# Optimization experiments

Measured on AMD Instinct MI355X. Metric: run time of the kernel, lower is better.

The kernel has to match this reference:

```python
import jax, jax.numpy as jnp
import numpy as np

S = 128           # seq_len
B = 256           # input_bits (bits per token, also neurons per head)
H = 16            # num_heads
NB = 12           # n_bits_per_neuron -> LUT size 2^12
PB = 7            # relative-position bits = ceil(log2(max_seq_len))
HEAD_IN = 2 * B + PB   # concat(query, key, rel_pos_bits) = 519
THRESH = H // 2


def setup_inputs() -> dict:
    key = jax.random.key(0)
    k1, k2, k3 = jax.random.split(key, 3)
    tokens = jax.random.randint(k1, (S, B), 0, 2, dtype=jnp.int32)           # binary token bits
    memory = jax.random.normal(k2, (H, B, 2 ** NB), dtype=jnp.float32)       # RAM LUT contents per head/neuron
    connections = jax.random.randint(k3, (H, B, NB), 0, HEAD_IN, dtype=jnp.int32)  # per-neuron input-bit wiring
    return {"tokens": tokens, "memory": memory, "connections": connections}


def reference(tokens, memory, connections):
    idx = jnp.arange(S)
    rel = idx[:, None] - idx[None, :]                         # [S,S] i - j
    mask = (rel >= 0).astype(jnp.int32)                        # causal mask (j <= i)
    relc = jnp.clip(rel, 0, S - 1)
    # relative-distance binary encoding, LSB first: [S,S,PB]
    pos_bits = ((relc[..., None] >> jnp.arange(PB)) & 1).astype(jnp.int32)
    q = jnp.broadcast_to(tokens[:, None, :], (S, S, B))
    k = jnp.broadcast_to(tokens[None, :, :], (S, S, B))
    head_in = jnp.concatenate([q, k, pos_bits], axis=-1)       # [S,S,HEAD_IN]
    # RAM address per (query i, key j, head h, neuron n): pack NB wired bits, LSB first
    addr = jnp.zeros((S, S, H, B), dtype=jnp.int32)
    for b in range(NB):  # tiny fixed loop over bit planes, fully vectorized over S,S,H,B
        addr = addr + (head_in[..., connections[:, :, b]] << b)
    # LUT gather: memory[h, n, addr] -> [S,S,H,B]
    h_idx = jnp.arange(H)[:, None]
    n_idx = jnp.arange(B)[None, :]
    vals = memory[h_idx, n_idx, addr]
    bits = (vals > 0.0).astype(jnp.int32)                      # RAM neuron output bit
    # XOR accumulation over attended keys == masked sum mod 2: [S,H,B]
    head_res = jnp.sum(bits * mask[:, :, None, None], axis=1) % 2
    # majority vote across heads per bit
    ones_count = jnp.sum(head_res, axis=1)                     # [S,B]
    return (ones_count > THRESH).astype(jnp.int32)
```

## Files before the change

### kernel.cpp

```cpp
#include <hip/hip_runtime.h>


#define S 128
#define B 256
#define H 16
#define NB 12

__device__ __forceinline__ unsigned sig(unsigned x) {
    return x ^ ((x >> 3) & 0x70u) ^ ((x >> 6) & 0x70u);
}

#define TW(c) ((((c) & 3) << 1) + ((c) >> 7))
#define TP(c) (((c) >> 2) & 31)

__global__ __launch_bounds__(256) void pack_kernel(
    const int* __restrict__ tokens,
    unsigned* __restrict__ tokP)
{
    const int wid  = threadIdx.x >> 6;
    const int lane = threadIdx.x & 63;
    const int4* tp = (const int4*)tokens;
    #pragma unroll
    for (int r = 0; r < 4; ++r) {
        int i = blockIdx.x * 16 + wid * 4 + r;
        int4 x = tp[i * 64 + lane];
        unsigned long long B0 = __ballot((x.x & 1) != 0);
        unsigned long long B1 = __ballot((x.y & 1) != 0);
        unsigned long long B2 = __ballot((x.z & 1) != 0);
        unsigned long long B3 = __ballot((x.w & 1) != 0);
        int c = lane >> 1;
        unsigned long long s01 = (c & 1) ? B1 : B0;
        unsigned long long s23 = (c & 1) ? B3 : B2;
        unsigned long long s   = (c & 2) ? s23 : s01;
        unsigned word = (lane & 1) ? (unsigned)(s >> 32) : (unsigned)s;
        if (lane < 8) tokP[lane * 128 + i] = word;
    }
}

__global__ __launch_bounds__(256, 8) void softram_kernel(
    const unsigned* __restrict__ tokP,
    const float* __restrict__ memory,
    const int* __restrict__ connections,
    unsigned long long* __restrict__ pres)
{
    const int tid  = threadIdx.x;
    const int wid  = tid >> 6;
    const int rs   = wid >> 1;
    const int sub  = wid & 1;
    const int r    = blockIdx.x * 2 + rs;
    const int lane = tid & 63;

    __shared__ __align__(16) unsigned char      bytetab[2][4096];
    __shared__ __align__(16) unsigned int       tokT[8 * S];
    __shared__ __align__(16) unsigned short     akT[2][S];
    __shared__ __align__(16) unsigned short     apt[2][S];
    __shared__ __align__(16) unsigned short     aqs[2][S];
    __shared__ __align__(16) unsigned long long wsh[2][64];
    __shared__ unsigned long long baseS[2];
    __shared__ unsigned long long fbu[2];

    unsigned char* __restrict__ bt = bytetab[rs];

    const float4* mp = (const float4*)(memory + ((size_t)r << 12));
    float4 va[4];
    #pragma unroll
    for (int t = 0; t < 4; ++t) va[t] = mp[lane + 64 * (sub * 8 + t)];

    int c_l = (lane < NB) ? connections[(size_t)r * NB + lane] : 0;
    int cb[NB];
    #pragma unroll
    for (int b = 0; b < NB; ++b)
        cb[b] = __builtin_amdgcn_readfirstlane(__shfl(c_l, b));

    unsigned qmask = 0, kmask = 0, pmask = 0;
    #pragma unroll
    for (int b = 0; b < NB; ++b) {
        qmask |= (unsigned)(cb[b] < 256) << b;
        kmask |= (unsigned)(cb[b] >= 256 && cb[b] < 512) << b;
        pmask |= (unsigned)(cb[b] >= 512) << b;
    }
    const int qb = __popc(qmask);
    const int kb = __popc(kmask);
    const bool fast = (pmask == 0);

    ((int4*)tokT)[tid] = ((const int4*)tokP)[tid];
    __syncthreads();

    const int ii = sub * 64 + lane;
    unsigned qcls = 0;
    if (fast) {
        unsigned qc = 0, kc = 0;
        int qn = 0, kn = 0;
        #pragma unroll
        for (int b = 0; b < NB; ++b) {
            int c = cb[b];
            if (c < 256) {
                qc |= ((tokT[TW(c) * S + ii] >> TP(c)) & 1u) << qn;
                ++qn;
            } else {
                int c2 = c - 256;
                kc |= ((tokT[TW(c2) * S + ii] >> TP(c2)) & 1u) << kn;
                ++kn;
            }
        }
        akT[rs][ii] = (unsigned short)kc;
        qcls = qc;
    } else {
        unsigned aq = 0, ak = 0, ap = 0;
        #pragma unroll
        for (int b = 0; b < NB; ++b) {
            int c = cb[b];
            if (c < 256) {
                aq |= ((tokT[TW(c) * S + ii] >> TP(c)) & 1u) << b;
            } else if (c < 512) {
                int c2 = c - 256;
                ak |= ((tokT[TW(c2) * S + ii] >> TP(c2)) & 1u) << b;
            } else {
                ap |= (((unsigned)ii >> (c - 512)) & 1u) << b;
            }
        }
        akT[rs][ii] = (unsigned short)sig(ak);
        apt[rs][ii] = (unsigned short)sig(ap);
        aqs[rs][ii] = (unsigned short)sig(aq);
        qcls = sig(aq);
    }

    #pragma unroll
    for (int t = 0; t < 8; ++t) {
        float4 v = va[t & 3];
        if (t + 4 < 8) va[t & 3] = mp[lane + 64 * (sub * 8 + t + 4)];
        unsigned w = (unsigned)(v.x > 0.f)
                   | ((unsigned)(v.y > 0.f) << 8)
                   | ((unsigned)(v.z > 0.f) << 16)
                   | ((unsigned)(v.w > 0.f) << 24);
        *(unsigned*)&bt[sig(4u * (unsigned)(lane + 64 * (sub * 8 + t)))] = w;
    }
    __syncthreads();

    unsigned long long rpart = 0;
    unsigned long long Wfull = 0;
    unsigned long long Vreg  = 0;
    unsigned Creg = 0;
    unsigned acc_fb = 0;

    if (fast) {
        const bool formA = (qb <= 6);
        const int SBITS  = formA ? qb : kb;
        unsigned apl = 0, aul = 0;
        {
            int scnt = 0, lcnt = 0;
            #pragma unroll
            for (int b = 0; b < NB; ++b) {
                int c = cb[b];
                bool isS = formA ? (c < 256) : (c >= 256);
                if (isS) {
                    apl |= (((unsigned)lane >> scnt) & 1u) << b;
                    ++scnt;
                } else {
                    int p = SBITS + lcnt;
                    if (p < 6) apl |= (((unsigned)lane >> p) & 1u) << b;
                    else       aul |= (((unsigned)lane >> (p - 6)) & 1u) << b;
                    ++lcnt;
                }
            }
        }
        const unsigned spl  = sig(apl);
        const unsigned saul = sig(aul);
        unsigned Wlo = 0, Whi = 0;
        #pragma unroll 8
        for (int k = 0; k < 32; ++k) {
            int it = sub * 32 + k;
            unsigned sau  = (unsigned)__builtin_amdgcn_readlane((int)saul, it);
            unsigned bitv = bt[sau ^ spl] & 1u;
            unsigned long long Bm = __ballot(bitv != 0u);
            Wlo = (lane == it) ? (unsigned)Bm : Wlo;
            Whi = (lane == it) ? (unsigned)(Bm >> 32) : Whi;
        }
        if ((lane >> 5) == sub)
            wsh[rs][lane] = ((unsigned long long)Whi << 32) | Wlo;
    } else {
        if (sub == 0) {
            const unsigned aqv0 = qcls;
            const unsigned aqvU = aqs[rs][64 + lane];
            unsigned acc0 = 0, accP = 0;
            for (int s8 = 0; s8 < 8; ++s8) {
                uint4 uk = *(const uint4*)&akT[rs][s8 * 8];
                #pragma unroll
                for (int t = 0; t < 8; ++t) {
                    int j = s8 * 8 + t;
                    unsigned w = ((const unsigned*)&uk)[t >> 1];
                    unsigned akv = (w >> ((t & 1) * 16)) & 0xffffu;
                    int d0 = lane - j;
                    unsigned v0 = bt[aqv0 ^ akv ^ (unsigned)apt[rs][d0 & 127]] & 1u;
                    acc0 ^= (d0 >= 0) ? v0 : 0u;
                    int d1 = lane + 64 - j;
                    unsigned v1 = bt[aqvU ^ akv ^ (unsigned)apt[rs][d1]] & 1u;
                    accP ^= v1;
                }
            }
            rpart = __ballot(acc0 != 0u);
            unsigned long long up = __ballot(accP != 0u);
            if (lane == 0) fbu[rs] = up;
        } else {
            const unsigned aqv1 = qcls;
            unsigned acc1 = 0;
            for (int s8 = 8; s8 < 16; ++s8) {
                uint4 uk = *(const uint4*)&akT[rs][s8 * 8];
                #pragma unroll
                for (int t = 0; t < 8; ++t) {
                    int j = s8 * 8 + t;
                    unsigned w = ((const unsigned*)&uk)[t >> 1];
                    unsigned akv = (w >> ((t & 1) * 16)) & 0xffffu;
                    int d1 = lane + 64 - j;
                    unsigned v1 = bt[aqv1 ^ akv ^ (unsigned)apt[rs][d1 & 127]] & 1u;
                    acc1 ^= (d1 >= 0) ? v1 : 0u;
                }
            }
            acc_fb = acc1;
        }
    }
    __syncthreads();

    if (fast) {
        Wfull = wsh[rs][lane];
        const bool formA = (qb <= 6);
        if (formA) {
            unsigned kcls = akT[rs][ii];
            unsigned g0 = kcls << qb;
            unsigned long long V = __shfl(Wfull, (int)(g0 >> 6)) >> (g0 & 63u);
            #pragma unroll
            for (int d = 1; d < 64; d <<= 1) {
                unsigned long long u = __shfl_up(V, (unsigned)d);
                V ^= (lane >= d) ? u : 0ull;
            }
            if (sub == 0) {
                rpart = __ballot(((V >> qcls) & 1ull) != 0ull);
                unsigned long long Ab = __shfl(V, 63);
                if (lane == 0) baseS[rs] = Ab;
            } else {
                Vreg = V;
            }
        } else {
            unsigned kcls = akT[rs][ii];
            unsigned C = 1u << kcls;
            #pragma unroll
            for (int d = 1; d < 64; d <<= 1) {
                unsigned u = __shfl_up(C, (unsigned)d);
                C ^= (lane >= d) ? u : 0u;
            }
            if (sub == 0) {
                unsigned g0a = qcls << kb;
                unsigned W0 = (unsigned)(__shfl(Wfull, (int)(g0a >> 6)) >> (g0a & 63u));
                rpart = __ballot((__popc(W0 & C) & 1) != 0);
                unsigned Cb = __shfl(C, 63);
                if (lane == 0) baseS[rs] = (unsigned long long)Cb;
            } else {
                Creg = C;
            }
        }
    } else if (sub == 1) {
        unsigned long long up = fbu[rs];
        acc_fb ^= (unsigned)((up >> lane) & 1ull);
        rpart = __ballot(acc_fb != 0u);
    }
    __syncthreads();

    if (fast && sub == 1) {
        const bool formA = (qb <= 6);
        if (formA) {
            unsigned long long V1 = Vreg ^ baseS[rs];
            rpart = __ballot(((V1 >> qcls) & 1ull) != 0ull);
        } else {
            unsigned C1 = Creg ^ (unsigned)baseS[rs];
            unsigned g0b = qcls << kb;
            unsigned W1 = (unsigned)(__shfl(Wfull, (int)(g0b >> 6)) >> (g0b & 63u));
            rpart = __ballot((__popc(W1 & C1) & 1) != 0);
        }
    }

    if (lane == 0) pres[(size_t)r * 2 + sub] = rpart;
}

__global__ __launch_bounds__(128) void vote_kernel(
    const unsigned long long* __restrict__ pres,
    int* __restrict__ out)
{
    const int n = blockIdx.x;
    const int i = threadIdx.x;
    const int w = i >> 6, b = i & 63;
    int tot = 0;
    #pragma unroll
    for (int h = 0; h < H; ++h)
        tot += (int)((pres[(size_t)(h * 256 + n) * 2 + w] >> b) & 1ull);
    out[i * B + n] = (tot > (H / 2)) ? 1 : 0;
}

extern "C" void kernel_launch(void* const* d_in, const int* in_sizes, int n_in,
                              void* d_out, int out_size, void* d_ws, size_t ws_size,
                              hipStream_t stream) {
    const int*   tokens      = (const int*)d_in[0];
    const float* memory      = (const float*)d_in[1];
    const int*   connections = (const int*)d_in[2];
    int*         out         = (int*)d_out;
    unsigned long long* pres = (unsigned long long*)d_ws;
    unsigned*           tokP = (unsigned*)((char*)d_ws + (64u << 10));
    (void)in_sizes; (void)n_in; (void)out_size; (void)ws_size;

    pack_kernel<<<8, 256, 0, stream>>>(tokens, tokP);
    softram_kernel<<<2048, 256, 0, stream>>>(tokP, memory, connections, pres);
    vote_kernel<<<B, 128, 0, stream>>>(pres, out);
}
```

Baseline: 108.3 us.

## Process two neuron pairs per block with upfront prefetch and LDS-only barriers

Each softram block now handles four neurons (two per wave pair, processed one after the other), so the grid is halved. The tokT staging and its setup are amortised over twice the work. Both neurons' LUT float4 data and connection lists are loaded up front, so the second neuron's global loads overlap the first neuron's compute. __syncthreads is replaced by a barrier that waits only on LDS/scalar counters. The cost is more VGPRs for the 16 prefetched float4s and lower occupancy, since launch bounds drop from 8 to 4 waves per EU.

New measurement: 111.6 us. 1.03x slower.

```diff
diff --git a/kernel.cpp b/kernel.cpp
--- a/kernel.cpp
+++ b/kernel.cpp
@@ -12,6 +12,12 @@
 
 #define TW(c) ((((c) & 3) << 1) + ((c) >> 7))
 #define TP(c) (((c) >> 2) & 31)
+
+#define LGKM_BAR() do { \
+    asm volatile("s_waitcnt lgkmcnt(0)" ::: "memory"); \
+    __builtin_amdgcn_s_barrier(); \
+    __builtin_amdgcn_sched_barrier(0); \
+} while (0)
 
 __global__ __launch_bounds__(256) void pack_kernel(
     const int* __restrict__ tokens,
@@ -37,7 +43,7 @@
     }
 }
 
-__global__ __launch_bounds__(256, 8) void softram_kernel(
+__global__ __launch_bounds__(256, 4) void softram_kernel(
     const unsigned* __restrict__ tokP,
     const float* __restrict__ memory,
     const int* __restrict__ connections,
@@ -47,8 +53,10 @@
     const int wid  = tid >> 6;
     const int rs   = wid >> 1;
     const int sub  = wid & 1;
-    const int r    = blockIdx.x * 2 + rs;
     const int lane = tid & 63;
+    const int r0   = blockIdx.x * 4 + rs;
+    const int r1   = blockIdx.x * 4 + 2 + rs;
+    const int ii   = sub * 64 + lane;
 
     __shared__ __align__(16) unsigned char      bytetab[2][4096];
     __shared__ __align__(16) unsigned int       tokT[8 * S];
@@ -59,226 +67,234 @@
     __shared__ unsigned long long baseS[2];
     __shared__ unsigned long long fbu[2];
 
-    unsigned char* __restrict__ bt = bytetab[rs];
-
-    const float4* mp = (const float4*)(memory + ((size_t)r << 12));
-    float4 va[4];
+    int cl0 = (lane < NB) ? connections[(size_t)r0 * NB + lane] : 0;
+    int cl1 = (lane < NB) ? connections[(size_t)r1 * NB + lane] : 0;
+    int4 tk = ((const int4*)tokP)[tid];
+
+    const float4* mp0 = (const float4*)(memory + ((size_t)r0 << 12));
+    const float4* mp1 = (const float4*)(memory + ((size_t)r1 << 12));
+    float4 va0[8], va1[8];
     #pragma unroll
-    for (int t = 0; t < 4; ++t) va[t] = mp[lane + 64 * (sub * 8 + t)];
-
-    int c_l = (lane < NB) ? connections[(size_t)r * NB + lane] : 0;
-    int cb[NB];
+    for (int t = 0; t < 8; ++t) va0[t] = mp0[lane + 64 * (sub * 8 + t)];
     #pragma unroll
-    for (int b = 0; b < NB; ++b)
-        cb[b] = __builtin_amdgcn_readfirstlane(__shfl(c_l, b));
-
-    unsigned qmask = 0, kmask = 0, pmask = 0;
-    #pragma unroll
-    for (int b = 0; b < NB; ++b) {
-        qmask |= (unsigned)(cb[b] < 256) << b;
-        kmask |= (unsigned)(cb[b] >= 256 && cb[b] < 512) << b;
-        pmask |= (unsigned)(cb[b] >= 512) << b;
-    }
-    const int qb = __popc(qmask);
-    const int kb = __popc(kmask);
-    const bool fast = (pmask == 0);
-
-    ((int4*)tokT)[tid] = ((const int4*)tokP)[tid];
-    __syncthreads();
-
-    const int ii = sub * 64 + lane;
-    unsigned qcls = 0;
-    if (fast) {
-        unsigned qc = 0, kc = 0;
-        int qn = 0, kn = 0;
+    for (int t = 0; t < 8; ++t) va1[t] = mp1[lane + 64 * (sub * 8 + t)];
+
+    ((int4*)tokT)[tid] = tk;
+    LGKM_BAR();
+
+    auto do_gen = [&](int r, float4 (&va)[8], int c_l) {
+        unsigned char* __restrict__ bt = bytetab[rs];
+
+        int cb[NB];
+        #pragma unroll
+        for (int b = 0; b < NB; ++b)
+            cb[b] = __builtin_amdgcn_readfirstlane(__shfl(c_l, b));
+        unsigned qmask = 0, kmask = 0, pmask = 0;
         #pragma unroll
         for (int b = 0; b < NB; ++b) {
-            int c = cb[b];
-            if (c < 256) {
-                qc |= ((tokT[TW(c) * S + ii] >> TP(c)) & 1u) << qn;
-                ++qn;
-            } else {
-                int c2 = c - 256;
-                kc |= ((tokT[TW(c2) * S + ii] >> TP(c2)) & 1u) << kn;
-                ++kn;
-            }
-        }
-        akT[rs][ii] = (unsigned short)kc;
-        qcls = qc;
-    } else {
-        unsigned aq = 0, ak = 0, ap = 0;
-        #pragma unroll
-        for (int b = 0; b < NB; ++b) {
-            int c = cb[b];
-            if (c < 256) {
-                aq |= ((tokT[TW(c) * S + ii] >> TP(c)) & 1u) << b;
-            } else if (c < 512) {
-                int c2 = c - 256;
-                ak |= ((tokT[TW(c2) * S + ii] >> TP(c2)) & 1u) << b;
-            } else {
-                ap |= (((unsigned)ii >> (c - 512)) & 1u) << b;
-            }
-        }
-        akT[rs][ii] = (unsigned short)sig(ak);
-        apt[rs][ii] = (unsigned short)sig(ap);
-        aqs[rs][ii] = (unsigned short)sig(aq);
-        qcls = sig(aq);
-    }
-
-    #pragma unroll
-    for (int t = 0; t < 8; ++t) {
-        float4 v = va[t & 3];
-        if (t + 4 < 8) va[t & 3] = mp[lane + 64 * (sub * 8 + t + 4)];
-        unsigned w = (unsigned)(v.x > 0.f)
-                   | ((unsigned)(v.y > 0.f) << 8)
-                   | ((unsigned)(v.z > 0.f) << 16)
-                   | ((unsigned)(v.w > 0.f) << 24);
-        *(unsigned*)&bt[sig(4u * (unsigned)(lane + 64 * (sub * 8 + t)))] = w;
-    }
-    __syncthreads();
-
-    unsigned long long rpart = 0;
-    unsigned long long Wfull = 0;
-    unsigned long long Vreg  = 0;
-    unsigned Creg = 0;
-    unsigned acc_fb = 0;
-
-    if (fast) {
-        const bool formA = (qb <= 6);
-        const int SBITS  = formA ? qb : kb;
-        unsigned apl = 0, aul = 0;
-        {
-            int scnt = 0, lcnt = 0;
+            qmask |= (unsigned)(cb[b] < 256) << b;
+            kmask |= (unsigned)(cb[b] >= 256 && cb[b] < 512) << b;
+            pmask |= (unsigned)(cb[b] >= 512) << b;
+        }
+        const int qb = __popc(qmask);
+        const int kb = __popc(kmask);
+        const bool fast = (pmask == 0);
+
+        unsigned qcls = 0;
+        if (fast) {
+            unsigned qc = 0, kc = 0;
+            int qn = 0, kn = 0;
             #pragma unroll
             for (int b = 0; b < NB; ++b) {
                 int c = cb[b];
-                bool isS = formA ? (c < 256) : (c >= 256);
-                if (isS) {
-                    apl |= (((unsigned)lane >> scnt) & 1u) << b;
-                    ++scnt;
+                if (c < 256) {
+                    qc |= ((tokT[TW(c) * S + ii] >> TP(c)) & 1u) << qn;
+                    ++qn;
                 } else {
-                    int p = SBITS + lcnt;
-                    if (p < 6) apl |= (((unsigned)lane >> p) & 1u) << b;
-                    else       aul |= (((unsigned)lane >> (p - 6)) & 1u) << b;
-                    ++lcnt;
-                }
-            }
-        }
-        const unsigned spl  = sig(apl);
-        const unsigned saul = sig(aul);
-        unsigned Wlo = 0, Whi = 0;
-        #pragma unroll 8
-        for (int k = 0; k < 32; ++k) {
-            int it = sub * 32 + k;
-            unsigned sau  = (unsigned)__builtin_amdgcn_readlane((int)saul, it);
-            unsigned bitv = bt[sau ^ spl] & 1u;
-            unsigned long long Bm = __ballot(bitv != 0u);
-            Wlo = (lane == it) ? (unsigned)Bm : Wlo;
-            Whi = (lane == it) ? (unsigned)(Bm >> 32) : Whi;
-        }
-        if ((lane >> 5) == sub)
-            wsh[rs][lane] = ((unsigned long long)Whi << 32) | Wlo;
-    } else {
-        if (sub == 0) {
-            const unsigned aqv0 = qcls;
-            const unsigned aqvU = aqs[rs][64 + lane];
-            unsigned acc0 = 0, accP = 0;
-            for (int s8 = 0; s8 < 8; ++s8) {
-                uint4 uk = *(const uint4*)&akT[rs][s8 * 8];
+                    int c2 = c - 256;
+                    kc |= ((tokT[TW(c2) * S + ii] >> TP(c2)) & 1u) << kn;
+                    ++kn;
+                }
+            }
+            akT[rs][ii] = (unsigned short)kc;
+            qcls = qc;
+        } else {
+            unsigned aq = 0, ak = 0, ap = 0;
+            #pragma unroll
+            for (int b = 0; b < NB; ++b) {
+                int c = cb[b];
+                if (c < 256) {
+                    aq |= ((tokT[TW(c) * S + ii] >> TP(c)) & 1u) << b;
+                } else if (c < 512) {
+                    int c2 = c - 256;
+                    ak |= ((tokT[TW(c2) * S + ii] >> TP(c2)) & 1u) << b;
+                } else {
+                    ap |= (((unsigned)ii >> (c - 512)) & 1u) << b;
+                }
+            }
+            akT[rs][ii] = (unsigned short)sig(ak);
+            apt[rs][ii] = (unsigned short)sig(ap);
+            aqs[rs][ii] = (unsigned short)sig(aq);
+            qcls = sig(aq);
+        }
+
+        #pragma unroll
+        for (int t = 0; t < 8; ++t) {
+            float4 v = va[t];
+            unsigned w = (unsigned)(v.x > 0.f)
+                       | ((unsigned)(v.y > 0.f) << 8)
+                       | ((unsigned)(v.z > 0.f) << 16)
+                       | ((unsigned)(v.w > 0.f) << 24);
+            *(unsigned*)&bt[sig(4u * (unsigned)(lane + 64 * (sub * 8 + t)))] = w;
+        }
+        LGKM_BAR();
+
+        unsigned long long rpart = 0;
+        unsigned long long Wfull = 0;
+        unsigned long long Vreg  = 0;
+        unsigned Creg = 0;
+        unsigned acc_fb = 0;
+
+        if (fast) {
+            const bool formA = (qb <= 6);
+            const int SBITS  = formA ? qb : kb;
+            unsigned apl = 0, aul = 0;
+            {
+                int scnt = 0, lcnt = 0;
                 #pragma unroll
-                for (int t = 0; t < 8; ++t) {
-                    int j = s8 * 8 + t;
-                    unsigned w = ((const unsigned*)&uk)[t >> 1];
-                    unsigned akv = (w >> ((t & 1) * 16)) & 0xffffu;
-                    int d0 = lane - j;
-                    unsigned v0 = bt[aqv0 ^ akv ^ (unsigned)apt[rs][d0 & 127]] & 1u;
-                    acc0 ^= (d0 >= 0) ? v0 : 0u;
-                    int d1 = lane + 64 - j;
-                    unsigned v1 = bt[aqvU ^ akv ^ (unsigned)apt[rs][d1]] & 1u;
-                    accP ^= v1;
-                }
-            }
-            rpart = __ballot(acc0 != 0u);
-            unsigned long long up = __ballot(accP != 0u);
-            if (lane == 0) fbu[rs] = up;
+                for (int b = 0; b < NB; ++b) {
+                    int c = cb[b];
+                    bool isS = formA ? (c < 256) : (c >= 256);
+                    if (isS) {
+                        apl |= (((unsigned)lane >> scnt) & 1u) << b;
+                        ++scnt;
+                    } else {
+                        int p = SBITS + lcnt;
+                        if (p < 6) apl |= (((unsigned)lane >> p) & 1u) << b;
+                        else       aul |= (((unsigned)lane >> (p - 6)) & 1u) << b;
+                        ++lcnt;
+                    }
+                }
+            }
+            const unsigned spl  = sig(apl);
+            const unsigned saul = sig(aul);
+            unsigned Wlo = 0, Whi = 0;
+            #pragma unroll 8
+            for (int k = 0; k < 32; ++k) {
+                int it = sub * 32 + k;
+                unsigned sau  = (unsigned)__builtin_amdgcn_readlane((int)saul, it);
+                unsigned bitv = bt[sau ^ spl] & 1u;
+                unsigned long long Bm = __ballot(bitv != 0u);
+                Wlo = (lane == it) ? (unsigned)Bm : Wlo;
+                Whi = (lane == it) ? (unsigned)(Bm >> 32) : Whi;
+            }
+            if ((lane >> 5) == sub)
+                wsh[rs][lane] = ((unsigned long long)Whi << 32) | Wlo;
         } else {
-            const unsigned aqv1 = qcls;
-            unsigned acc1 = 0;
-            for (int s8 = 8; s8 < 16; ++s8) {
-                uint4 uk = *(const uint4*)&akT[rs][s8 * 8];
+            if (sub == 0) {
+                const unsigned aqv0 = qcls;
+                const unsigned aqvU = aqs[rs][64 + lane];
+                unsigned acc0 = 0, accP = 0;
+                for (int s8 = 0; s8 < 8; ++s8) {
+                    uint4 uk = *(const uint4*)&akT[rs][s8 * 8];
+                    #pragma unroll
+                    for (int t = 0; t < 8; ++t) {
+                        int j = s8 * 8 + t;
+                        unsigned w = ((const unsigned*)&uk)[t >> 1];
+                        unsigned akv = (w >> ((t & 1) * 16)) & 0xffffu;
+                        int d0 = lane - j;
+                        unsigned v0 = bt[aqv0 ^ akv ^ (unsigned)apt[rs][d0 & 127]] & 1u;
+                        acc0 ^= (d0 >= 0) ? v0 : 0u;
+                        int d1 = lane + 64 - j;
+                        unsigned v1 = bt[aqvU ^ akv ^ (unsigned)apt[rs][d1]] & 1u;
+                        accP ^= v1;
+                    }
+                }
+                rpart = __ballot(acc0 != 0u);
+                unsigned long long up = __ballot(accP != 0u);
+                if (lane == 0) fbu[rs] = up;
+            } else {
+                const unsigned aqv1 = qcls;
+                unsigned acc1 = 0;
+                for (int s8 = 8; s8 < 16; ++s8) {
+                    uint4 uk = *(const uint4*)&akT[rs][s8 * 8];
+                    #pragma unroll
+                    for (int t = 0; t < 8; ++t) {
+                        int j = s8 * 8 + t;
+                        unsigned w = ((const unsigned*)&uk)[t >> 1];
+                        unsigned akv = (w >> ((t & 1) * 16)) & 0xffffu;
+                        int d1 = lane + 64 - j;
+                        unsigned v1 = bt[aqv1 ^ akv ^ (unsigned)apt[rs][d1 & 127]] & 1u;
+                        acc1 ^= (d1 >= 0) ? v1 : 0u;
+                    }
+                }
+                acc_fb = acc1;
+            }
+        }
+        LGKM_BAR();
+
+        if (fast) {
+            Wfull = wsh[rs][lane];
+            const bool formA = (qb <= 6);
+            if (formA) {
+                unsigned kcls = akT[rs][ii];
+                unsigned g0 = kcls << qb;
+                unsigned long long V = __shfl(Wfull, (int)(g0 >> 6)) >> (g0 & 63u);
                 #pragma unroll
-                for (int t = 0; t < 8; ++t) {
-                    int j = s8 * 8 + t;
-                    unsigned w = ((const unsigned*)&uk)[t >> 1];
-                    unsigned akv = (w >> ((t & 1) * 16)) & 0xffffu;
-                    int d1 = lane + 64 - j;
-                    unsigned v1 = bt[aqv1 ^ akv ^ (unsigned)apt[rs][d1 & 127]] & 1u;
-                    acc1 ^= (d1 >= 0) ? v1 : 0u;
-                }
-            }
-            acc_fb = acc1;
-        }
-    }
-    __syncthreads();
-
-    if (fast) {
-        Wfull = wsh[rs][lane];
-        const bool formA = (qb <= 6);
-        if (formA) {
-            unsigned kcls = akT[rs][ii];
-            unsigned g0 = kcls << qb;
-            unsigned long long V = __shfl(Wfull, (int)(g0 >> 6)) >> (g0 & 63u);
-            #pragma unroll
-            for (int d = 1; d < 64; d <<= 1) {
-                unsigned long long u = __shfl_up(V, (unsigned)d);
-                V ^= (lane >= d) ? u : 0ull;
-            }
-            if (sub == 0) {
-                rpart = __ballot(((V >> qcls) & 1ull) != 0ull);
-                unsigned long long Ab = __shfl(V, 63);
-                if (lane == 0) baseS[rs] = Ab;
+                for (int d = 1; d < 64; d <<= 1) {
+                    unsigned long long u = __shfl_up(V, (unsigned)d);
+                    V ^= (lane >= d) ? u : 0ull;
+                }
+                if (sub == 0) {
+                    rpart = __ballot(((V >> qcls) & 1ull) != 0ull);
+                    unsigned long long Ab = __shfl(V, 63);
+                    if (lane == 0) baseS[rs] = Ab;
+                } else {
+                    Vreg = V;
+                }
             } else {
-                Vreg = V;
-            }
-        } else {
-            unsigned kcls = akT[rs][ii];
-            unsigned C = 1u << kcls;
-            #pragma unroll
-            for (int d = 1; d < 64; d <<= 1) {
-                unsigned u = __shfl_up(C, (unsigned)d);
-                C ^= (lane >= d) ? u : 0u;
-            }
-            if (sub == 0) {
-                unsigned g0a = qcls << kb;
-                unsigned W0 = (unsigned)(__shfl(Wfull, (int)(g0a >> 6)) >> (g0a & 63u));
-                rpart = __ballot((__popc(W0 & C) & 1) != 0);
-                unsigned Cb = __shfl(C, 63);
-                if (lane == 0) baseS[rs] = (unsigned long long)Cb;
+                unsigned kcls = akT[rs][ii];
+                unsigned C = 1u << kcls;
+                #pragma unroll
+                for (int d = 1; d < 64; d <<= 1) {
+                    unsigned u = __shfl_up(C, (unsigned)d);
+                    C ^= (lane >= d) ? u : 0u;
+                }
+                if (sub == 0) {
+                    unsigned g0a = qcls << kb;
+                    unsigned W0 = (unsigned)(__shfl(Wfull, (int)(g0a >> 6)) >> (g0a & 63u));
+                    rpart = __ballot((__popc(W0 & C) & 1) != 0);
+                    unsigned Cb = __shfl(C, 63);
+                    if (lane == 0) baseS[rs] = (unsigned long long)Cb;
+                } else {
+                    Creg = C;
+                }
+            }
+        } else if (sub == 1) {
+            unsigned long long up = fbu[rs];
+            acc_fb ^= (unsigned)((up >> lane) & 1ull);
+            rpart = __ballot(acc_fb != 0u);
+        }
+        LGKM_BAR();
+
+        if (fast && sub == 1) {
+            const bool formA = (qb <= 6);
+            if (formA) {
+                unsigned long long V1 = Vreg ^ baseS[rs];
+                rpart = __ballot(((V1 >> qcls) & 1ull) != 0ull);
             } else {
-                Creg = C;
-            }
-        }
-    } else if (sub == 1) {
-        unsigned long long up = fbu[rs];
-        acc_fb ^= (unsigned)((up >> lane) & 1ull);
-        rpart = __ballot(acc_fb != 0u);
-    }
-    __syncthreads();
-
-    if (fast && sub == 1) {
-        const bool formA = (qb <= 6);
-        if (formA) {
-            unsigned long long V1 = Vreg ^ baseS[rs];
-            rpart = __ballot(((V1 >> qcls) & 1ull) != 0ull);
-        } else {
-            unsigned C1 = Creg ^ (unsigned)baseS[rs];
-            unsigned g0b = qcls << kb;
-            unsigned W1 = (unsigned)(__shfl(Wfull, (int)(g0b >> 6)) >> (g0b & 63u));
-            rpart = __ballot((__popc(W1 & C1) & 1) != 0);
-        }
-    }
-
-    if (lane == 0) pres[(size_t)r * 2 + sub] = rpart;
+                unsigned C1 = Creg ^ (unsigned)baseS[rs];
+                unsigned g0b = qcls << kb;
+                unsigned W1 = (unsigned)(__shfl(Wfull, (int)(g0b >> 6)) >> (g0b & 63u));
+                rpart = __ballot((__popc(W1 & C1) & 1) != 0);
+            }
+        }
+
+        if (lane == 0) pres[(size_t)r * 2 + sub] = rpart;
+    };
+
+    do_gen(r0, va0, cl0);
+    do_gen(r1, va1, cl1);
 }
 
 __global__ __launch_bounds__(128) void vote_kernel(
@@ -307,6 +323,6 @@
     (void)in_sizes; (void)n_in; (void)out_size; (void)ws_size;
 
     pack_kernel<<<8, 256, 0, stream>>>(tokens, tokP);
-    softram_kernel<<<2048, 256, 0, stream>>>(tokP, memory, connections, pres);
+    softram_kernel<<<1024, 256, 0, stream>>>(tokP, memory, connections, pres);
     vote_kernel<<<B, 128, 0, stream>>>(pres, out);
 }
```
